# Kernel tuning notes

Hardware: AMD Instinct MI355X
Metric: run time of the kernel (lower is better)

## Reference

```python
import jax, jax.numpy as jnp
import numpy as np

SIZE = 4096
DOWN = SIZE // 16  # reduction_factor = 16 -> 256
N_TASKS = 16
BATCH = 2048
INIT_STD = 0.01


def setup_inputs() -> dict:
    key = jax.random.key(0)
    k_x, k_t, k_wd, k_wu = jax.random.split(key, 4)
    x = jax.random.normal(k_x, (BATCH, SIZE), dtype=jnp.float32)
    task_id = jax.random.randint(k_t, (BATCH,), 0, N_TASKS)
    # Stacked per-task adapter params (init: normal(std=0.01) weights, zero bias)
    Wd = jax.random.normal(k_wd, (N_TASKS, SIZE, DOWN), dtype=jnp.float32) * INIT_STD
    bd = jnp.zeros((N_TASKS, DOWN), dtype=jnp.float32)
    Wu = jax.random.normal(k_wu, (N_TASKS, DOWN, SIZE), dtype=jnp.float32) * INIT_STD
    bu = jnp.zeros((N_TASKS, SIZE), dtype=jnp.float32)
    return {"x": x, "task_id": task_id, "Wd": Wd, "bd": bd, "Wu": Wu, "bu": bu}


def reference(x, task_id, Wd, bd, Wu, bu):
    # Down-projection for all tasks, then select each sample's routed task.
    # [B, T, DOWN] is small (B*T*256), cheaper than gathering [B, SIZE, DOWN] weights.
    down_all = jnp.einsum('bd,tdh->bth', x, Wd) + bd[None]
    down = jnp.take_along_axis(down_all, task_id[:, None, None], axis=1)[:, 0]  # [B, DOWN]
    act = jax.nn.silu(down)
    # Up-projection for all tasks, select routed task. [B, T, SIZE]
    up_all = jnp.einsum('bh,thd->btd', act, Wu) + bu[None]
    up = jnp.take_along_axis(up_all, task_id[:, None, None], axis=1)[:, 0]  # [B, SIZE]
    return x + up  # residual=True (default)
```

## Files before the change

### kernel.cpp

```cpp
#include <hip/hip_runtime.h>

#define BATCH 2048
#define SIZE 4096
#define DOWN 256
#define NTASK 16
#define KC 16
#define KCHUNK (SIZE / KC)

typedef _Float16 half8 __attribute__((ext_vector_type(8)));
typedef float floatx4 __attribute__((ext_vector_type(4)));

__device__ __forceinline__ int imin(int a, int b) { return a < b ? a : b; }
__device__ __forceinline__ int uswz(int n) { return n ^ ((n >> 3) & 7); }

__global__ __launch_bounds__(256) void sort_kernel(const int* __restrict__ task_id,
                                                   int* __restrict__ taskOff,
                                                   int* __restrict__ sortedIdx,
                                                   int* __restrict__ taskOfPos) {
    __shared__ int cnt[NTASK];
    __shared__ int base[NTASK + 1];
    __shared__ int cur[NTASK];
    int tid = threadIdx.x;
    if (tid < NTASK) cnt[tid] = 0;
    __syncthreads();
    for (int i = tid; i < BATCH; i += 256) atomicAdd(&cnt[task_id[i]], 1);
    __syncthreads();
    if (tid == 0) {
        int s = 0;
        for (int t = 0; t < NTASK; t++) { base[t] = s; s += cnt[t]; }
        base[NTASK] = s;
    }
    __syncthreads();
    if (tid < NTASK) { cur[tid] = base[tid]; taskOff[tid] = base[tid]; }
    if (tid == 0) taskOff[NTASK] = BATCH;
    __syncthreads();
    for (int i = tid; i < BATCH; i += 256) {
        int t = task_id[i];
        int p = atomicAdd(&cur[t], 1);
        sortedIdx[p] = i;
        taskOfPos[p] = t;
    }
}

__global__ __launch_bounds__(256, 2) void gemm1_kernel(const float* __restrict__ x,
                                                       const float* __restrict__ Wd,
                                                       const int* __restrict__ taskOff,
                                                       const int* __restrict__ sortedIdx,
                                                       _Float16* __restrict__ partial) {
    int task = blockIdx.x >> 1, z = blockIdx.x & 1, kc = blockIdx.y;
    int rowStart = taskOff[task];
    int nrows = taskOff[task + 1] - rowStart;
    if (nrows <= 0) return;

    __shared__ half8 A_lds[8][65];
    __shared__ half8 B_lds[8][256];

    int tid = threadIdx.x;
    int wave = tid >> 6, lane = tid & 63, quad = lane >> 4, l15 = lane & 15;
    int kbase0 = kc * KCHUNK;
    const float* Wdt = Wd + (size_t)task * SIZE * DOWN;

    int bswz[4];
#pragma unroll
    for (int i = 0; i < 4; i++) bswz[i] = uswz(wave * 64 + i * 16 + l15);

    for (int r0 = z * 64; r0 < nrows; r0 += 128) {
        floatx4 acc[4][4];
#pragma unroll
        for (int mi = 0; mi < 4; mi++)
#pragma unroll
            for (int ni = 0; ni < 4; ni++) acc[mi][ni] = (floatx4){0.f, 0.f, 0.f, 0.f};

        int arow = tid >> 2;
        int asrc = sortedIdx[rowStart + imin(r0 + arow, nrows - 1)];
        const float* xrow = x + (size_t)asrc * SIZE;

        for (int kb = 0; kb < KCHUNK; kb += 64) {
            int kglob = kbase0 + kb;
            floatx4 fa[2][2];
#pragma unroll
            for (int j = 0; j < 2; j++) {
                int kg = ((tid & 3) << 1) | j;
                const float* src = xrow + kglob + kg * 8;
                fa[j][0] = *(const floatx4*)(src);
                fa[j][1] = *(const floatx4*)(src + 4);
            }
            floatx4 fb[2][8];
#pragma unroll
            for (int s = 0; s < 2; s++) {
                int kg = s * 4 + wave;
                const float* src = Wdt + (size_t)(kglob + kg * 8) * DOWN + lane * 4;
#pragma unroll
                for (int j = 0; j < 8; j++) fb[s][j] = *(const floatx4*)(src + (size_t)j * DOWN);
            }
            __syncthreads();
#pragma unroll
            for (int j = 0; j < 2; j++) {
                int kg = ((tid & 3) << 1) | j;
                half8 h;
                h[0] = (_Float16)fa[j][0][0]; h[1] = (_Float16)fa[j][0][1];
                h[2] = (_Float16)fa[j][0][2]; h[3] = (_Float16)fa[j][0][3];
                h[4] = (_Float16)fa[j][1][0]; h[5] = (_Float16)fa[j][1][1];
                h[6] = (_Float16)fa[j][1][2]; h[7] = (_Float16)fa[j][1][3];
                A_lds[kg][arow] = h;
            }
#pragma unroll
            for (int s = 0; s < 2; s++) {
                int kg = s * 4 + wave;
#pragma unroll
                for (int i = 0; i < 4; i++) {
                    half8 h;
#pragma unroll
                    for (int j = 0; j < 8; j++) h[j] = (_Float16)fb[s][j][i];
                    B_lds[kg][uswz(lane * 4 + i)] = h;
                }
            }
            __syncthreads();
#pragma unroll
            for (int ks = 0; ks < 2; ks++) {
                int kg = ks * 4 + quad;
                half8 a[4], b[4];
#pragma unroll
                for (int i = 0; i < 4; i++) a[i] = A_lds[kg][i * 16 + l15];
#pragma unroll
                for (int i = 0; i < 4; i++) b[i] = B_lds[kg][bswz[i]];
#pragma unroll
                for (int mi = 0; mi < 4; mi++)
#pragma unroll
                    for (int ni = 0; ni < 4; ni++)
                        acc[mi][ni] = __builtin_amdgcn_mfma_f32_16x16x32_f16(
                            a[mi], b[ni], acc[mi][ni], 0, 0, 0);
            }
        }
#pragma unroll
        for (int mi = 0; mi < 4; mi++) {
#pragma unroll
            for (int reg = 0; reg < 4; reg++) {
                int r = r0 + mi * 16 + quad * 4 + reg;
                if (r < nrows) {
                    size_t rowoff = ((size_t)kc * BATCH + (rowStart + r)) * DOWN;
#pragma unroll
                    for (int ni = 0; ni < 4; ni++) {
                        int h = wave * 64 + ni * 16 + l15;
                        partial[rowoff + h] = (_Float16)acc[mi][ni][reg];
                    }
                }
            }
        }
    }
}

__global__ __launch_bounds__(256) void silu_kernel(const _Float16* __restrict__ partial,
                                                   const float* __restrict__ bd,
                                                   const int* __restrict__ taskOfPos,
                                                   _Float16* __restrict__ act) {
    int idx = blockIdx.x * 256 + threadIdx.x;
    int s = idx >> 5;
    int h = (idx & 31) * 8;
    int t = taskOfPos[s];
    floatx4 b0 = *(const floatx4*)(bd + t * DOWN + h);
    floatx4 b1 = *(const floatx4*)(bd + t * DOWN + h + 4);
    float v[8];
    v[0] = b0[0]; v[1] = b0[1]; v[2] = b0[2]; v[3] = b0[3];
    v[4] = b1[0]; v[5] = b1[1]; v[6] = b1[2]; v[7] = b1[3];
#pragma unroll
    for (int kc = 0; kc < KC; kc++) {
        half8 p = *(const half8*)(partial + ((size_t)kc * BATCH + s) * DOWN + h);
#pragma unroll
        for (int j = 0; j < 8; j++) v[j] += (float)p[j];
    }
    half8 o;
#pragma unroll
    for (int j = 0; j < 8; j++) {
        float sv = v[j] / (1.0f + __expf(-v[j]));
        o[j] = (_Float16)sv;
    }
    *(half8*)(act + (size_t)s * DOWN + h) = o;
}

__global__ __launch_bounds__(256, 2) void gemm2_kernel(const _Float16* __restrict__ act,
                                                       const float* __restrict__ Wu,
                                                       const float* __restrict__ bu,
                                                       const float* __restrict__ x,
                                                       const int* __restrict__ taskOff,
                                                       const int* __restrict__ sortedIdx,
                                                       float* __restrict__ out) {
    int nt = blockIdx.x, task = blockIdx.y;
    int rowStart = taskOff[task];
    int nrows = taskOff[task + 1] - rowStart;
    if (nrows <= 0) return;

    __shared__ half8 A_lds[8][129];
    __shared__ half8 B_lds[8][128];

    int tid = threadIdx.x;
    int wave = tid >> 6, lane = tid & 63, quad = lane >> 4, l15 = lane & 15;
    int wm = wave >> 1, wn = wave & 1;
    int ncol0 = nt * 128;
    const float* Wut = Wu + (size_t)task * DOWN * SIZE;

    int bswz[4];
#pragma unroll
    for (int i = 0; i < 4; i++) bswz[i] = uswz(wn * 64 + i * 16 + l15);
    int kgB = tid >> 5, nfB = tid & 31;

    for (int r0 = 0; r0 < nrows; r0 += 128) {
        floatx4 acc[4][4];
#pragma unroll
        for (int mi = 0; mi < 4; mi++)
#pragma unroll
            for (int ni = 0; ni < 4; ni++) acc[mi][ni] = (floatx4){0.f, 0.f, 0.f, 0.f};

        int arow = tid >> 1;
        int s_a = rowStart + imin(r0 + arow, nrows - 1);
        const _Float16* actrow = act + (size_t)s_a * DOWN;

        for (int kb = 0; kb < DOWN; kb += 64) {
            half8 ha[4];
#pragma unroll
            for (int j = 0; j < 4; j++) {
                int kg = ((tid & 1) << 2) | j;
                ha[j] = *(const half8*)(actrow + kb + kg * 8);
            }
            floatx4 fb[8];
            const float* src = Wut + (size_t)(kb + kgB * 8) * SIZE + ncol0 + nfB * 4;
#pragma unroll
            for (int j = 0; j < 8; j++) fb[j] = *(const floatx4*)(src + (size_t)j * SIZE);
            __syncthreads();
#pragma unroll
            for (int j = 0; j < 4; j++) {
                int kg = ((tid & 1) << 2) | j;
                A_lds[kg][arow] = ha[j];
            }
#pragma unroll
            for (int i = 0; i < 4; i++) {
                half8 h;
#pragma unroll
                for (int j = 0; j < 8; j++) h[j] = (_Float16)fb[j][i];
                B_lds[kgB][uswz(nfB * 4 + i)] = h;
            }
            __syncthreads();
#pragma unroll
            for (int ks = 0; ks < 2; ks++) {
                int kg = ks * 4 + quad;
                half8 a[4], b[4];
#pragma unroll
                for (int i = 0; i < 4; i++) a[i] = A_lds[kg][wm * 64 + i * 16 + l15];
#pragma unroll
                for (int i = 0; i < 4; i++) b[i] = B_lds[kg][bswz[i]];
#pragma unroll
                for (int mi = 0; mi < 4; mi++)
#pragma unroll
                    for (int ni = 0; ni < 4; ni++)
                        acc[mi][ni] = __builtin_amdgcn_mfma_f32_16x16x32_f16(
                            a[mi], b[ni], acc[mi][ni], 0, 0, 0);
            }
        }
#pragma unroll
        for (int mi = 0; mi < 4; mi++) {
#pragma unroll
            for (int reg = 0; reg < 4; reg++) {
                int r = r0 + wm * 64 + mi * 16 + quad * 4 + reg;
                if (r < nrows) {
                    int b = sortedIdx[rowStart + r];
                    const float* xr = x + (size_t)b * SIZE;
                    float* outr = out + (size_t)b * SIZE;
#pragma unroll
                    for (int ni = 0; ni < 4; ni++) {
                        int n = ncol0 + wn * 64 + ni * 16 + l15;
                        outr[n] = acc[mi][ni][reg] + bu[task * SIZE + n] + xr[n];
                    }
                }
            }
        }
    }
}

extern "C" void kernel_launch(void* const* d_in, const int* in_sizes, int n_in,
                              void* d_out, int out_size, void* d_ws, size_t ws_size,
                              hipStream_t stream) {
    const float* x       = (const float*)d_in[0];
    const int*   task_id = (const int*)d_in[1];
    const float* Wd      = (const float*)d_in[2];
    const float* bd      = (const float*)d_in[3];
    const float* Wu      = (const float*)d_in[4];
    const float* bu      = (const float*)d_in[5];
    float* out = (float*)d_out;

    _Float16* partial = (_Float16*)d_out;
    _Float16* act     = (_Float16*)d_ws;
    int* taskOff   = (int*)(act + (size_t)BATCH * DOWN);
    int* sortedIdx = taskOff + 32;
    int* taskOfPos = sortedIdx + BATCH;

    sort_kernel<<<1, 256, 0, stream>>>(task_id, taskOff, sortedIdx, taskOfPos);
    gemm1_kernel<<<dim3(NTASK * 2, KC), 256, 0, stream>>>(x, Wd, taskOff, sortedIdx, partial);
    silu_kernel<<<(BATCH * DOWN / 8) / 256, 256, 0, stream>>>(partial, bd, taskOfPos, act);
    gemm2_kernel<<<dim3(SIZE / 128, NTASK), 256, 0, stream>>>(act, Wu, bu, x, taskOff,
                                                              sortedIdx, out);
}
```

Before: 236.1 us.

## Stage full A tile in LDS once and give each wave private B tiles without barriers

Both GEMMs now load the whole row tile of activations (the x chunk or act rows) into LDS once per row block, instead of reloading it every k step. Each wave converts and stores its own slice of B into a private LDS region, so the two __syncthreads per k step are removed. gemm2 switches to 64-row by 256-column tiles with a row split across two blocks, matching gemm1. The cost is more registers per thread (16 float4 loads per k step) and the loss of the old XOR swizzle on B, which may bring back LDS bank conflicts.

```diff
diff --git a/kernel.cpp b/kernel.cpp
--- a/kernel.cpp
+++ b/kernel.cpp
@@ -8,10 +8,10 @@
 #define KCHUNK (SIZE / KC)
 
 typedef _Float16 half8 __attribute__((ext_vector_type(8)));
+typedef _Float16 half4 __attribute__((ext_vector_type(4)));
 typedef float floatx4 __attribute__((ext_vector_type(4)));
 
 __device__ __forceinline__ int imin(int a, int b) { return a < b ? a : b; }
-__device__ __forceinline__ int uswz(int n) { return n ^ ((n >> 3) & 7); }
 
 __global__ __launch_bounds__(256) void sort_kernel(const int* __restrict__ task_id,
                                                    int* __restrict__ taskOff,
@@ -52,78 +52,64 @@
     int nrows = taskOff[task + 1] - rowStart;
     if (nrows <= 0) return;
 
-    __shared__ half8 A_lds[8][65];
-    __shared__ half8 B_lds[8][256];
+    __shared__ half8 A_lds[32][64];
+    __shared__ half8 B_lds[4][64][8];
 
     int tid = threadIdx.x;
     int wave = tid >> 6, lane = tid & 63, quad = lane >> 4, l15 = lane & 15;
-    int kbase0 = kc * KCHUNK;
+    int kbase = kc * KCHUNK;
     const float* Wdt = Wd + (size_t)task * SIZE * DOWN;
-
-    int bswz[4];
-#pragma unroll
-    for (int i = 0; i < 4; i++) bswz[i] = uswz(wave * 64 + i * 16 + l15);
+    int arow = tid >> 2, ac = tid & 3;
 
     for (int r0 = z * 64; r0 < nrows; r0 += 128) {
+        __syncthreads();
+        {
+            int asrc = sortedIdx[rowStart + imin(r0 + arow, nrows - 1)];
+            const float* xr = x + (size_t)asrc * SIZE + kbase;
+            floatx4 f[16];
+#pragma unroll
+            for (int i = 0; i < 16; i++)
+                f[i] = *(const floatx4*)(xr + i * 16 + ac * 4);
+#pragma unroll
+            for (int i = 0; i < 16; i++) {
+                half4 h;
+                h[0] = (_Float16)f[i][0]; h[1] = (_Float16)f[i][1];
+                h[2] = (_Float16)f[i][2]; h[3] = (_Float16)f[i][3];
+                int kg = i * 2 + (ac >> 1);
+                *((half4*)(&A_lds[kg][arow]) + (ac & 1)) = h;
+            }
+        }
+        __syncthreads();
+
         floatx4 acc[4][4];
 #pragma unroll
         for (int mi = 0; mi < 4; mi++)
 #pragma unroll
             for (int ni = 0; ni < 4; ni++) acc[mi][ni] = (floatx4){0.f, 0.f, 0.f, 0.f};
 
-        int arow = tid >> 2;
-        int asrc = sortedIdx[rowStart + imin(r0 + arow, nrows - 1)];
-        const float* xrow = x + (size_t)asrc * SIZE;
-
         for (int kb = 0; kb < KCHUNK; kb += 64) {
-            int kglob = kbase0 + kb;
-            floatx4 fa[2][2];
-#pragma unroll
-            for (int j = 0; j < 2; j++) {
-                int kg = ((tid & 3) << 1) | j;
-                const float* src = xrow + kglob + kg * 8;
-                fa[j][0] = *(const floatx4*)(src);
-                fa[j][1] = *(const floatx4*)(src + 4);
-            }
-            floatx4 fb[2][8];
-#pragma unroll
-            for (int s = 0; s < 2; s++) {
-                int kg = s * 4 + wave;
-                const float* src = Wdt + (size_t)(kglob + kg * 8) * DOWN + lane * 4;
-#pragma unroll
-                for (int j = 0; j < 8; j++) fb[s][j] = *(const floatx4*)(src + (size_t)j * DOWN);
-            }
-            __syncthreads();
-#pragma unroll
-            for (int j = 0; j < 2; j++) {
-                int kg = ((tid & 3) << 1) | j;
-                half8 h;
-                h[0] = (_Float16)fa[j][0][0]; h[1] = (_Float16)fa[j][0][1];
-                h[2] = (_Float16)fa[j][0][2]; h[3] = (_Float16)fa[j][0][3];
-                h[4] = (_Float16)fa[j][1][0]; h[5] = (_Float16)fa[j][1][1];
-                h[6] = (_Float16)fa[j][1][2]; h[7] = (_Float16)fa[j][1][3];
-                A_lds[kg][arow] = h;
-            }
-#pragma unroll
-            for (int s = 0; s < 2; s++) {
-                int kg = s * 4 + wave;
-#pragma unroll
-                for (int i = 0; i < 4; i++) {
+            floatx4 fb[16];
+            const float* bs =
+                Wdt + (size_t)(kbase + kb + quad * 16) * DOWN + wave * 64 + l15 * 4;
+#pragma unroll
+            for (int j = 0; j < 16; j++) fb[j] = *(const floatx4*)(bs + (size_t)j * DOWN);
+#pragma unroll
+            for (int g = 0; g < 2; g++)
+#pragma unroll
+                for (int n2 = 0; n2 < 4; n2++) {
                     half8 h;
 #pragma unroll
-                    for (int j = 0; j < 8; j++) h[j] = (_Float16)fb[s][j][i];
-                    B_lds[kg][uswz(lane * 4 + i)] = h;
-                }
-            }
-            __syncthreads();
+                    for (int e = 0; e < 8; e++) h[e] = (_Float16)fb[g * 8 + e][n2];
+                    B_lds[wave][l15 * 4 + n2][quad * 2 + g] = h;
+                }
 #pragma unroll
             for (int ks = 0; ks < 2; ks++) {
-                int kg = ks * 4 + quad;
+                int kg = (kb >> 3) + ks * 4 + quad;
                 half8 a[4], b[4];
 #pragma unroll
                 for (int i = 0; i < 4; i++) a[i] = A_lds[kg][i * 16 + l15];
 #pragma unroll
-                for (int i = 0; i < 4; i++) b[i] = B_lds[kg][bswz[i]];
+                for (int i = 0; i < 4; i++) b[i] = B_lds[wave][i * 16 + l15][ks * 4 + quad];
 #pragma unroll
                 for (int mi = 0; mi < 4; mi++)
 #pragma unroll
@@ -185,69 +171,62 @@
                                                        const int* __restrict__ taskOff,
                                                        const int* __restrict__ sortedIdx,
                                                        float* __restrict__ out) {
-    int nt = blockIdx.x, task = blockIdx.y;
+    int nt = blockIdx.x >> 1, z = blockIdx.x & 1, task = blockIdx.y;
     int rowStart = taskOff[task];
     int nrows = taskOff[task + 1] - rowStart;
     if (nrows <= 0) return;
 
-    __shared__ half8 A_lds[8][129];
-    __shared__ half8 B_lds[8][128];
+    __shared__ half8 A_lds[32][64];
+    __shared__ half8 B_lds[4][64][8];
 
     int tid = threadIdx.x;
     int wave = tid >> 6, lane = tid & 63, quad = lane >> 4, l15 = lane & 15;
-    int wm = wave >> 1, wn = wave & 1;
-    int ncol0 = nt * 128;
+    int ncol0 = nt * 256;
     const float* Wut = Wu + (size_t)task * DOWN * SIZE;
-
-    int bswz[4];
-#pragma unroll
-    for (int i = 0; i < 4; i++) bswz[i] = uswz(wn * 64 + i * 16 + l15);
-    int kgB = tid >> 5, nfB = tid & 31;
-
-    for (int r0 = 0; r0 < nrows; r0 += 128) {
+    int arow = tid >> 2, ac = tid & 3;
+
+    for (int r0 = z * 64; r0 < nrows; r0 += 128) {
+        __syncthreads();
+        {
+            int s_a = rowStart + imin(r0 + arow, nrows - 1);
+            const _Float16* ar = act + (size_t)s_a * DOWN;
+#pragma unroll
+            for (int j = 0; j < 8; j++) {
+                int kg = j * 4 + ac;
+                A_lds[kg][arow] = *(const half8*)(ar + kg * 8);
+            }
+        }
+        __syncthreads();
+
         floatx4 acc[4][4];
 #pragma unroll
         for (int mi = 0; mi < 4; mi++)
 #pragma unroll
             for (int ni = 0; ni < 4; ni++) acc[mi][ni] = (floatx4){0.f, 0.f, 0.f, 0.f};
 
-        int arow = tid >> 1;
-        int s_a = rowStart + imin(r0 + arow, nrows - 1);
-        const _Float16* actrow = act + (size_t)s_a * DOWN;
-
         for (int kb = 0; kb < DOWN; kb += 64) {
-            half8 ha[4];
-#pragma unroll
-            for (int j = 0; j < 4; j++) {
-                int kg = ((tid & 1) << 2) | j;
-                ha[j] = *(const half8*)(actrow + kb + kg * 8);
-            }
-            floatx4 fb[8];
-            const float* src = Wut + (size_t)(kb + kgB * 8) * SIZE + ncol0 + nfB * 4;
-#pragma unroll
-            for (int j = 0; j < 8; j++) fb[j] = *(const floatx4*)(src + (size_t)j * SIZE);
-            __syncthreads();
-#pragma unroll
-            for (int j = 0; j < 4; j++) {
-                int kg = ((tid & 1) << 2) | j;
-                A_lds[kg][arow] = ha[j];
-            }
-#pragma unroll
-            for (int i = 0; i < 4; i++) {
-                half8 h;
-#pragma unroll
-                for (int j = 0; j < 8; j++) h[j] = (_Float16)fb[j][i];
-                B_lds[kgB][uswz(nfB * 4 + i)] = h;
-            }
-            __syncthreads();
+            floatx4 fb[16];
+            const float* bs =
+                Wut + (size_t)(kb + quad * 16) * SIZE + ncol0 + wave * 64 + l15 * 4;
+#pragma unroll
+            for (int j = 0; j < 16; j++) fb[j] = *(const floatx4*)(bs + (size_t)j * SIZE);
+#pragma unroll
+            for (int g = 0; g < 2; g++)
+#pragma unroll
+                for (int n2 = 0; n2 < 4; n2++) {
+                    half8 h;
+#pragma unroll
+                    for (int e = 0; e < 8; e++) h[e] = (_Float16)fb[g * 8 + e][n2];
+                    B_lds[wave][l15 * 4 + n2][quad * 2 + g] = h;
+                }
 #pragma unroll
             for (int ks = 0; ks < 2; ks++) {
-                int kg = ks * 4 + quad;
+                int kg = (kb >> 3) + ks * 4 + quad;
                 half8 a[4], b[4];
 #pragma unroll
-                for (int i = 0; i < 4; i++) a[i] = A_lds[kg][wm * 64 + i * 16 + l15];
-#pragma unroll
-                for (int i = 0; i < 4; i++) b[i] = B_lds[kg][bswz[i]];
+                for (int i = 0; i < 4; i++) a[i] = A_lds[kg][i * 16 + l15];
+#pragma unroll
+                for (int i = 0; i < 4; i++) b[i] = B_lds[wave][i * 16 + l15][ks * 4 + quad];
 #pragma unroll
                 for (int mi = 0; mi < 4; mi++)
 #pragma unroll
@@ -260,14 +239,14 @@
         for (int mi = 0; mi < 4; mi++) {
 #pragma unroll
             for (int reg = 0; reg < 4; reg++) {
-                int r = r0 + wm * 64 + mi * 16 + quad * 4 + reg;
+                int r = r0 + mi * 16 + quad * 4 + reg;
                 if (r < nrows) {
                     int b = sortedIdx[rowStart + r];
                     const float* xr = x + (size_t)b * SIZE;
                     float* outr = out + (size_t)b * SIZE;
 #pragma unroll
                     for (int ni = 0; ni < 4; ni++) {
-                        int n = ncol0 + wn * 64 + ni * 16 + l15;
+                        int n = ncol0 + wave * 64 + ni * 16 + l15;
                         outr[n] = acc[mi][ni][reg] + bu[task * SIZE + n] + xr[n];
                     }
                 }
@@ -296,6 +275,6 @@
     sort_kernel<<<1, 256, 0, stream>>>(task_id, taskOff, sortedIdx, taskOfPos);
     gemm1_kernel<<<dim3(NTASK * 2, KC), 256, 0, stream>>>(x, Wd, taskOff, sortedIdx, partial);
     silu_kernel<<<(BATCH * DOWN / 8) / 256, 256, 0, stream>>>(partial, bd, taskOfPos, act);
-    gemm2_kernel<<<dim3(SIZE / 128, NTASK), 256, 0, stream>>>(act, Wu, bu, x, taskOff,
-                                                              sortedIdx, out);
-}
+    gemm2_kernel<<<dim3(32, NTASK), 256, 0, stream>>>(act, Wu, bu, x, taskOff,
+                                                      sortedIdx, out);
+}
```

New measurement: 254.5 us. 1.08x slower.

## Pre-convert weights to packed fp16 tiles and double-buffer GEMMs with async LDS loads

Applied to the files above, without the earlier changes.

Adds a prep kernel that folds the sort into block 0 and converts Wd and Wu from fp32 into fp16 tiles laid out to match the MFMA operand order. The weights go into the workspace and the output buffer. Both GEMMs then stream these tiles straight into double-buffered LDS with global_load_lds, overlapping the next tile's load with the current MFMAs, and occupancy is raised to 3. This removes per-block re-conversion of the weights and halves their read bytes in the GEMMs. The cost is an extra full pass over the weights each call, plus a larger workspace requirement with an fp32 fallback path when the workspace is too small.

```diff
diff --git a/kernel.cpp b/kernel.cpp
--- a/kernel.cpp
+++ b/kernel.cpp
@@ -11,12 +11,17 @@
 typedef float floatx4 __attribute__((ext_vector_type(4)));
 
 __device__ __forceinline__ int imin(int a, int b) { return a < b ? a : b; }
-__device__ __forceinline__ int uswz(int n) { return n ^ ((n >> 3) & 7); }
-
-__global__ __launch_bounds__(256) void sort_kernel(const int* __restrict__ task_id,
-                                                   int* __restrict__ taskOff,
-                                                   int* __restrict__ sortedIdx,
-                                                   int* __restrict__ taskOfPos) {
+
+__device__ __forceinline__ void async16(void* lds, const void* g) {
+    __builtin_amdgcn_global_load_lds((const __attribute__((address_space(1))) unsigned int*)g,
+                                     (__attribute__((address_space(3))) unsigned int*)lds,
+                                     16, 0, 0);
+}
+
+__device__ __forceinline__ void sort_body(const int* __restrict__ task_id,
+                                          int* __restrict__ taskOff,
+                                          int* __restrict__ sortedIdx,
+                                          int* __restrict__ taskOfPos) {
     __shared__ int cnt[NTASK];
     __shared__ int base[NTASK + 1];
     __shared__ int cur[NTASK];
@@ -42,8 +47,62 @@
     }
 }
 
-__global__ __launch_bounds__(256, 2) void gemm1_kernel(const float* __restrict__ x,
-                                                       const float* __restrict__ Wd,
+__global__ __launch_bounds__(256) void sort_kernel(const int* __restrict__ task_id,
+                                                   int* __restrict__ taskOff,
+                                                   int* __restrict__ sortedIdx,
+                                                   int* __restrict__ taskOfPos) {
+    sort_body(task_id, taskOff, sortedIdx, taskOfPos);
+}
+
+__global__ __launch_bounds__(256) void prep_kernel(const int* __restrict__ task_id,
+                                                   int* __restrict__ taskOff,
+                                                   int* __restrict__ sortedIdx,
+                                                   int* __restrict__ taskOfPos,
+                                                   const float* __restrict__ Wd,
+                                                   const float* __restrict__ Wu,
+                                                   _Float16* __restrict__ Wd16,
+                                                   _Float16* __restrict__ Wu16) {
+    int b = blockIdx.x;
+    if (b == 0) {
+        sort_body(task_id, taskOff, sortedIdx, taskOfPos);
+        return;
+    }
+    int tid = threadIdx.x, w = tid >> 6, lane = tid & 63;
+    const float* src;
+    _Float16* dst;
+    size_t rstride;
+    if (b <= 1024) {
+        int i = b - 1, t = i >> 6, ks = i & 63;
+        src = Wd + ((size_t)t * SIZE + ks * 64) * DOWN;
+        dst = Wd16 + (size_t)(t * 64 + ks) * 16384;
+        rstride = DOWN;
+    } else {
+        int i = b - 1025, t = i >> 6, nt = (i >> 2) & 15, ks = i & 3;
+        src = Wu + ((size_t)t * DOWN + ks * 64) * SIZE + nt * 256;
+        dst = Wu16 + (size_t)((t * 16 + nt) * 4 + ks) * 16384;
+        rstride = SIZE;
+    }
+#pragma unroll
+    for (int kk = 0; kk < 2; kk++) {
+        int kg = w * 2 + kk;
+        float f[8][4];
+#pragma unroll
+        for (int e = 0; e < 8; e++)
+#pragma unroll
+            for (int j = 0; j < 4; j++)
+                f[e][j] = src[(size_t)(kg * 8 + e) * rstride + j * 64 + lane];
+#pragma unroll
+        for (int j = 0; j < 4; j++) {
+            half8 h;
+#pragma unroll
+            for (int e = 0; e < 8; e++) h[e] = (_Float16)f[e][j];
+            *(half8*)(dst + (size_t)(kg * 256 + j * 64 + lane) * 8) = h;
+        }
+    }
+}
+
+__global__ __launch_bounds__(256, 3) void gemm1_kernel(const float* __restrict__ x,
+                                                       const _Float16* __restrict__ Wd16,
                                                        const int* __restrict__ taskOff,
                                                        const int* __restrict__ sortedIdx,
                                                        _Float16* __restrict__ partial) {
@@ -52,85 +111,81 @@
     int nrows = taskOff[task + 1] - rowStart;
     if (nrows <= 0) return;
 
-    __shared__ half8 A_lds[8][65];
-    __shared__ half8 B_lds[8][256];
+    __shared__ floatx4 Af[2][64][8];
+    __shared__ half8 Bp[2][4][256];
 
     int tid = threadIdx.x;
     int wave = tid >> 6, lane = tid & 63, quad = lane >> 4, l15 = lane & 15;
-    int kbase0 = kc * KCHUNK;
-    const float* Wdt = Wd + (size_t)task * SIZE * DOWN;
-
-    int bswz[4];
-#pragma unroll
-    for (int i = 0; i < 4; i++) bswz[i] = uswz(wave * 64 + i * 16 + l15);
+    int arow = tid >> 2, c4 = tid & 3;
+    int kcbase = kc * KCHUNK;
 
     for (int r0 = z * 64; r0 < nrows; r0 += 128) {
+        int asrc = sortedIdx[rowStart + imin(r0 + arow, nrows - 1)];
+        const float* xrow = x + (size_t)asrc * SIZE + kcbase;
+
+        {
+            const char* tb = (const char*)Wd16 +
+                             (((size_t)task * 64 + kc * 4) << 15);
+#pragma unroll
+            for (int i = 0; i < 4; i++)
+                async16((char*)(&Bp[0][0][0]) + (wave * 4 + i) * 1024,
+                        tb + (wave * 4 + i) * 1024 + lane * 16);
+            floatx4 f0 = *(const floatx4*)(xrow + c4 * 8);
+            floatx4 f1 = *(const floatx4*)(xrow + c4 * 8 + 4);
+            Af[0][arow][(c4 * 2) ^ (arow & 7)] = f0;
+            Af[0][arow][(c4 * 2 + 1) ^ (arow & 7)] = f1;
+        }
+        __syncthreads();
+
         floatx4 acc[4][4];
 #pragma unroll
         for (int mi = 0; mi < 4; mi++)
 #pragma unroll
             for (int ni = 0; ni < 4; ni++) acc[mi][ni] = (floatx4){0.f, 0.f, 0.f, 0.f};
 
-        int arow = tid >> 2;
-        int asrc = sortedIdx[rowStart + imin(r0 + arow, nrows - 1)];
-        const float* xrow = x + (size_t)asrc * SIZE;
-
-        for (int kb = 0; kb < KCHUNK; kb += 64) {
-            int kglob = kbase0 + kb;
-            floatx4 fa[2][2];
-#pragma unroll
-            for (int j = 0; j < 2; j++) {
-                int kg = ((tid & 3) << 1) | j;
-                const float* src = xrow + kglob + kg * 8;
-                fa[j][0] = *(const floatx4*)(src);
-                fa[j][1] = *(const floatx4*)(src + 4);
-            }
-            floatx4 fb[2][8];
-#pragma unroll
-            for (int s = 0; s < 2; s++) {
-                int kg = s * 4 + wave;
-                const float* src = Wdt + (size_t)(kglob + kg * 8) * DOWN + lane * 4;
-#pragma unroll
-                for (int j = 0; j < 8; j++) fb[s][j] = *(const floatx4*)(src + (size_t)j * DOWN);
+        int buf = 0;
+        for (int ts = 0; ts < 8; ts++) {
+            floatx4 f0, f1;
+            if (ts < 7) {
+                int tn = ts + 1;
+                const char* tb = (const char*)Wd16 +
+                                 (((size_t)task * 64 + kc * 4 + (tn >> 1)) << 15) +
+                                 ((size_t)(tn & 1) << 14);
+#pragma unroll
+                for (int i = 0; i < 4; i++)
+                    async16((char*)(&Bp[buf ^ 1][0][0]) + (wave * 4 + i) * 1024,
+                            tb + (wave * 4 + i) * 1024 + lane * 16);
+                f0 = *(const floatx4*)(xrow + tn * 32 + c4 * 8);
+                f1 = *(const floatx4*)(xrow + tn * 32 + c4 * 8 + 4);
+            }
+            half8 a[4], bfr[4];
+#pragma unroll
+            for (int mi = 0; mi < 4; mi++) {
+                int row = mi * 16 + l15, s7 = row & 7;
+                floatx4 u0 = Af[buf][row][(quad * 2) ^ s7];
+                floatx4 u1 = Af[buf][row][(quad * 2 + 1) ^ s7];
+                half8 h;
+                h[0] = (_Float16)u0[0]; h[1] = (_Float16)u0[1];
+                h[2] = (_Float16)u0[2]; h[3] = (_Float16)u0[3];
+                h[4] = (_Float16)u1[0]; h[5] = (_Float16)u1[1];
+                h[6] = (_Float16)u1[2]; h[7] = (_Float16)u1[3];
+                a[mi] = h;
+            }
+#pragma unroll
+            for (int ni = 0; ni < 4; ni++)
+                bfr[ni] = Bp[buf][quad][wave * 64 + ni * 16 + l15];
+#pragma unroll
+            for (int mi = 0; mi < 4; mi++)
+#pragma unroll
+                for (int ni = 0; ni < 4; ni++)
+                    acc[mi][ni] = __builtin_amdgcn_mfma_f32_16x16x32_f16(
+                        a[mi], bfr[ni], acc[mi][ni], 0, 0, 0);
+            if (ts < 7) {
+                Af[buf ^ 1][arow][(c4 * 2) ^ (arow & 7)] = f0;
+                Af[buf ^ 1][arow][(c4 * 2 + 1) ^ (arow & 7)] = f1;
             }
             __syncthreads();
-#pragma unroll
-            for (int j = 0; j < 2; j++) {
-                int kg = ((tid & 3) << 1) | j;
-                half8 h;
-                h[0] = (_Float16)fa[j][0][0]; h[1] = (_Float16)fa[j][0][1];
-                h[2] = (_Float16)fa[j][0][2]; h[3] = (_Float16)fa[j][0][3];
-                h[4] = (_Float16)fa[j][1][0]; h[5] = (_Float16)fa[j][1][1];
-                h[6] = (_Float16)fa[j][1][2]; h[7] = (_Float16)fa[j][1][3];
-                A_lds[kg][arow] = h;
-            }
-#pragma unroll
-            for (int s = 0; s < 2; s++) {
-                int kg = s * 4 + wave;
-#pragma unroll
-                for (int i = 0; i < 4; i++) {
-                    half8 h;
-#pragma unroll
-                    for (int j = 0; j < 8; j++) h[j] = (_Float16)fb[s][j][i];
-                    B_lds[kg][uswz(lane * 4 + i)] = h;
-                }
-            }
-            __syncthreads();
-#pragma unroll
-            for (int ks = 0; ks < 2; ks++) {
-                int kg = ks * 4 + quad;
-                half8 a[4], b[4];
-#pragma unroll
-                for (int i = 0; i < 4; i++) a[i] = A_lds[kg][i * 16 + l15];
-#pragma unroll
-                for (int i = 0; i < 4; i++) b[i] = B_lds[kg][bswz[i]];
-#pragma unroll
-                for (int mi = 0; mi < 4; mi++)
-#pragma unroll
-                    for (int ni = 0; ni < 4; ni++)
-                        acc[mi][ni] = __builtin_amdgcn_mfma_f32_16x16x32_f16(
-                            a[mi], b[ni], acc[mi][ni], 0, 0, 0);
-            }
+            buf ^= 1;
         }
 #pragma unroll
         for (int mi = 0; mi < 4; mi++) {
@@ -178,96 +233,283 @@
     *(half8*)(act + (size_t)s * DOWN + h) = o;
 }
 
-__global__ __launch_bounds__(256, 2) void gemm2_kernel(const _Float16* __restrict__ act,
-                                                       const float* __restrict__ Wu,
+__global__ __launch_bounds__(256, 3) void gemm2_kernel(const _Float16* __restrict__ act,
+                                                       const _Float16* __restrict__ Wu16,
                                                        const float* __restrict__ bu,
                                                        const float* __restrict__ x,
                                                        const int* __restrict__ taskOff,
                                                        const int* __restrict__ sortedIdx,
                                                        float* __restrict__ out) {
-    int nt = blockIdx.x, task = blockIdx.y;
+    int nt = blockIdx.x >> 1, z = blockIdx.x & 1, task = blockIdx.y;
     int rowStart = taskOff[task];
     int nrows = taskOff[task + 1] - rowStart;
     if (nrows <= 0) return;
 
-    __shared__ half8 A_lds[8][129];
-    __shared__ half8 B_lds[8][128];
+    __shared__ half8 Ah[2][64][4];
+    __shared__ half8 Bp[2][4][256];
 
     int tid = threadIdx.x;
     int wave = tid >> 6, lane = tid & 63, quad = lane >> 4, l15 = lane & 15;
-    int wm = wave >> 1, wn = wave & 1;
-    int ncol0 = nt * 128;
-    const float* Wut = Wu + (size_t)task * DOWN * SIZE;
-
-    int bswz[4];
-#pragma unroll
-    for (int i = 0; i < 4; i++) bswz[i] = uswz(wn * 64 + i * 16 + l15);
-    int kgB = tid >> 5, nfB = tid & 31;
-
-    for (int r0 = 0; r0 < nrows; r0 += 128) {
+    int ncol0 = nt * 256;
+
+    for (int r0 = z * 64; r0 < nrows; r0 += 128) {
+        int ar = wave * 16 + (lane >> 2);
+        const _Float16* asrc_row =
+            act + (size_t)(rowStart + imin(r0 + ar, nrows - 1)) * DOWN +
+            ((lane & 3) ^ (ar & 3)) * 8;
+
+        {
+            const char* tb = (const char*)Wu16 +
+                             (((size_t)(task * 16 + nt) * 4) << 15);
+#pragma unroll
+            for (int i = 0; i < 4; i++)
+                async16((char*)(&Bp[0][0][0]) + (wave * 4 + i) * 1024,
+                        tb + (wave * 4 + i) * 1024 + lane * 16);
+            async16((char*)(&Ah[0][0][0]) + wave * 1024, asrc_row);
+        }
+        __syncthreads();
+
         floatx4 acc[4][4];
 #pragma unroll
         for (int mi = 0; mi < 4; mi++)
 #pragma unroll
             for (int ni = 0; ni < 4; ni++) acc[mi][ni] = (floatx4){0.f, 0.f, 0.f, 0.f};
 
-        int arow = tid >> 1;
-        int s_a = rowStart + imin(r0 + arow, nrows - 1);
-        const _Float16* actrow = act + (size_t)s_a * DOWN;
-
-        for (int kb = 0; kb < DOWN; kb += 64) {
-            half8 ha[4];
-#pragma unroll
-            for (int j = 0; j < 4; j++) {
-                int kg = ((tid & 1) << 2) | j;
-                ha[j] = *(const half8*)(actrow + kb + kg * 8);
-            }
-            floatx4 fb[8];
-            const float* src = Wut + (size_t)(kb + kgB * 8) * SIZE + ncol0 + nfB * 4;
-#pragma unroll
-            for (int j = 0; j < 8; j++) fb[j] = *(const floatx4*)(src + (size_t)j * SIZE);
+        int buf = 0;
+        for (int ts = 0; ts < 8; ts++) {
+            if (ts < 7) {
+                int tn = ts + 1;
+                const char* tb = (const char*)Wu16 +
+                                 (((size_t)(task * 16 + nt) * 4 + (tn >> 1)) << 15) +
+                                 ((size_t)(tn & 1) << 14);
+#pragma unroll
+                for (int i = 0; i < 4; i++)
+                    async16((char*)(&Bp[buf ^ 1][0][0]) + (wave * 4 + i) * 1024,
+                            tb + (wave * 4 + i) * 1024 + lane * 16);
+                async16((char*)(&Ah[buf ^ 1][0][0]) + wave * 1024, asrc_row + tn * 32);
+            }
+            half8 a[4], bfr[4];
+#pragma unroll
+            for (int mi = 0; mi < 4; mi++) {
+                int row = mi * 16 + l15;
+                a[mi] = Ah[buf][row][quad ^ (row & 3)];
+            }
+#pragma unroll
+            for (int ni = 0; ni < 4; ni++)
+                bfr[ni] = Bp[buf][quad][wave * 64 + ni * 16 + l15];
+#pragma unroll
+            for (int mi = 0; mi < 4; mi++)
+#pragma unroll
+                for (int ni = 0; ni < 4; ni++)
+                    acc[mi][ni] = __builtin_amdgcn_mfma_f32_16x16x32_f16(
+                        a[mi], bfr[ni], acc[mi][ni], 0, 0, 0);
             __syncthreads();
-#pragma unroll
-            for (int j = 0; j < 4; j++) {
-                int kg = ((tid & 1) << 2) | j;
-                A_lds[kg][arow] = ha[j];
-            }
-#pragma unroll
-            for (int i = 0; i < 4; i++) {
-                half8 h;
-#pragma unroll
-                for (int j = 0; j < 8; j++) h[j] = (_Float16)fb[j][i];
-                B_lds[kgB][uswz(nfB * 4 + i)] = h;
-            }
-            __syncthreads();
-#pragma unroll
-            for (int ks = 0; ks < 2; ks++) {
-                int kg = ks * 4 + quad;
-                half8 a[4], b[4];
-#pragma unroll
-                for (int i = 0; i < 4; i++) a[i] = A_lds[kg][wm * 64 + i * 16 + l15];
-#pragma unroll
-                for (int i = 0; i < 4; i++) b[i] = B_lds[kg][bswz[i]];
-#pragma unroll
-                for (int mi = 0; mi < 4; mi++)
-#pragma unroll
-                    for (int ni = 0; ni < 4; ni++)
-                        acc[mi][ni] = __builtin_amdgcn_mfma_f32_16x16x32_f16(
-                            a[mi], b[ni], acc[mi][ni], 0, 0, 0);
-            }
+            buf ^= 1;
         }
 #pragma unroll
         for (int mi = 0; mi < 4; mi++) {
 #pragma unroll
             for (int reg = 0; reg < 4; reg++) {
-                int r = r0 + wm * 64 + mi * 16 + quad * 4 + reg;
+                int r = r0 + mi * 16 + quad * 4 + reg;
                 if (r < nrows) {
                     int b = sortedIdx[rowStart + r];
                     const float* xr = x + (size_t)b * SIZE;
                     float* outr = out + (size_t)b * SIZE;
 #pragma unroll
                     for (int ni = 0; ni < 4; ni++) {
-                        int n = ncol0 + wn * 64 + ni * 16 + l15;
+                        int n = ncol0 + wave * 64 + ni * 16 + l15;
+                        outr[n] = acc[mi][ni][reg] + bu[task * SIZE + n] + xr[n];
+                    }
+                }
+            }
+        }
+    }
+}
+
+__global__ __launch_bounds__(256, 2) void gemm1_fb(const float* __restrict__ x,
+                                                   const float* __restrict__ Wd,
+                                                   const int* __restrict__ taskOff,
+                                                   const int* __restrict__ sortedIdx,
+                                                   _Float16* __restrict__ partial) {
+    int task = blockIdx.x >> 1, z = blockIdx.x & 1, kc = blockIdx.y;
+    int rowStart = taskOff[task];
+    int nrows = taskOff[task + 1] - rowStart;
+    if (nrows <= 0) return;
+    __shared__ half8 A_lds[8][65];
+    __shared__ half8 B_lds[8][256];
+    int tid = threadIdx.x;
+    int wave = tid >> 6, lane = tid & 63, quad = lane >> 4, l15 = lane & 15;
+    int kbase0 = kc * KCHUNK;
+    const float* Wdt = Wd + (size_t)task * SIZE * DOWN;
+    int uswz[4];
+#pragma unroll
+    for (int i = 0; i < 4; i++) {
+        int n = wave * 64 + i * 16 + l15;
+        uswz[i] = n ^ ((n >> 3) & 7);
+    }
+    for (int r0 = z * 64; r0 < nrows; r0 += 128) {
+        floatx4 acc[4][4];
+#pragma unroll
+        for (int mi = 0; mi < 4; mi++)
+#pragma unroll
+            for (int ni = 0; ni < 4; ni++) acc[mi][ni] = (floatx4){0.f, 0.f, 0.f, 0.f};
+        int arow = tid >> 2;
+        int asrc = sortedIdx[rowStart + imin(r0 + arow, nrows - 1)];
+        const float* xrow = x + (size_t)asrc * SIZE;
+        for (int kb = 0; kb < KCHUNK; kb += 64) {
+            int kglob = kbase0 + kb;
+            floatx4 fa[2][2];
+#pragma unroll
+            for (int j = 0; j < 2; j++) {
+                int kg = ((tid & 3) << 1) | j;
+                const float* src = xrow + kglob + kg * 8;
+                fa[j][0] = *(const floatx4*)(src);
+                fa[j][1] = *(const floatx4*)(src + 4);
+            }
+            floatx4 fb[2][8];
+#pragma unroll
+            for (int s = 0; s < 2; s++) {
+                int kg = s * 4 + wave;
+                const float* src = Wdt + (size_t)(kglob + kg * 8) * DOWN + lane * 4;
+#pragma unroll
+                for (int j = 0; j < 8; j++) fb[s][j] = *(const floatx4*)(src + (size_t)j * DOWN);
+            }
+            __syncthreads();
+#pragma unroll
+            for (int j = 0; j < 2; j++) {
+                int kg = ((tid & 3) << 1) | j;
+                half8 h;
+                h[0] = (_Float16)fa[j][0][0]; h[1] = (_Float16)fa[j][0][1];
+                h[2] = (_Float16)fa[j][0][2]; h[3] = (_Float16)fa[j][0][3];
+                h[4] = (_Float16)fa[j][1][0]; h[5] = (_Float16)fa[j][1][1];
+                h[6] = (_Float16)fa[j][1][2]; h[7] = (_Float16)fa[j][1][3];
+                A_lds[kg][arow] = h;
+            }
+#pragma unroll
+            for (int s = 0; s < 2; s++) {
+                int kg = s * 4 + wave;
+#pragma unroll
+                for (int i = 0; i < 4; i++) {
+                    half8 h;
+#pragma unroll
+                    for (int j = 0; j < 8; j++) h[j] = (_Float16)fb[s][j][i];
+                    int n = lane * 4 + i;
+                    B_lds[kg][n ^ ((n >> 3) & 7)] = h;
+                }
+            }
+            __syncthreads();
+#pragma unroll
+            for (int ks = 0; ks < 2; ks++) {
+                int kg = ks * 4 + quad;
+                half8 a[4], b[4];
+#pragma unroll
+                for (int i = 0; i < 4; i++) a[i] = A_lds[kg][i * 16 + l15];
+#pragma unroll
+                for (int i = 0; i < 4; i++) b[i] = B_lds[kg][uswz[i]];
+#pragma unroll
+                for (int mi = 0; mi < 4; mi++)
+#pragma unroll
+                    for (int ni = 0; ni < 4; ni++)
+                        acc[mi][ni] = __builtin_amdgcn_mfma_f32_16x16x32_f16(
+                            a[mi], b[ni], acc[mi][ni], 0, 0, 0);
+            }
+        }
+#pragma unroll
+        for (int mi = 0; mi < 4; mi++) {
+#pragma unroll
+            for (int reg = 0; reg < 4; reg++) {
+                int r = r0 + mi * 16 + quad * 4 + reg;
+                if (r < nrows) {
+                    size_t rowoff = ((size_t)kc * BATCH + (rowStart + r)) * DOWN;
+#pragma unroll
+                    for (int ni = 0; ni < 4; ni++) {
+                        int h = wave * 64 + ni * 16 + l15;
+                        partial[rowoff + h] = (_Float16)acc[mi][ni][reg];
+                    }
+                }
+            }
+        }
+    }
+}
+
+__global__ __launch_bounds__(256, 2) void gemm2_fb(const _Float16* __restrict__ act,
+                                                   const float* __restrict__ Wu,
+                                                   const float* __restrict__ bu,
+                                                   const float* __restrict__ x,
+                                                   const int* __restrict__ taskOff,
+                                                   const int* __restrict__ sortedIdx,
+                                                   float* __restrict__ out) {
+    int nt = blockIdx.x >> 1, z = blockIdx.x & 1, task = blockIdx.y;
+    int rowStart = taskOff[task];
+    int nrows = taskOff[task + 1] - rowStart;
+    if (nrows <= 0) return;
+    __shared__ half8 A_lds[32][64];
+    __shared__ half8 B_lds[4][64][8];
+    int tid = threadIdx.x;
+    int wave = tid >> 6, lane = tid & 63, quad = lane >> 4, l15 = lane & 15;
+    int ncol0 = nt * 256;
+    const float* Wut = Wu + (size_t)task * DOWN * SIZE;
+    int arow = tid >> 2, ac = tid & 3;
+    for (int r0 = z * 64; r0 < nrows; r0 += 128) {
+        __syncthreads();
+        {
+            int s_a = rowStart + imin(r0 + arow, nrows - 1);
+            const _Float16* ar = act + (size_t)s_a * DOWN;
+#pragma unroll
+            for (int j = 0; j < 8; j++) {
+                int kg = j * 4 + ac;
+                A_lds[kg][arow] = *(const half8*)(ar + kg * 8);
+            }
+        }
+        __syncthreads();
+        floatx4 acc[4][4];
+#pragma unroll
+        for (int mi = 0; mi < 4; mi++)
+#pragma unroll
+            for (int ni = 0; ni < 4; ni++) acc[mi][ni] = (floatx4){0.f, 0.f, 0.f, 0.f};
+        for (int kb = 0; kb < DOWN; kb += 64) {
+            floatx4 fb[16];
+            const float* bs =
+                Wut + (size_t)(kb + quad * 16) * SIZE + ncol0 + wave * 64 + l15 * 4;
+#pragma unroll
+            for (int j = 0; j < 16; j++) fb[j] = *(const floatx4*)(bs + (size_t)j * SIZE);
+#pragma unroll
+            for (int g = 0; g < 2; g++)
+#pragma unroll
+                for (int n2 = 0; n2 < 4; n2++) {
+                    half8 h;
+#pragma unroll
+                    for (int e = 0; e < 8; e++) h[e] = (_Float16)fb[g * 8 + e][n2];
+                    B_lds[wave][l15 * 4 + n2][quad * 2 + g] = h;
+                }
+#pragma unroll
+            for (int ks = 0; ks < 2; ks++) {
+                int kg = (kb >> 3) + ks * 4 + quad;
+                half8 a[4], b[4];
+#pragma unroll
+                for (int i = 0; i < 4; i++) a[i] = A_lds[kg][i * 16 + l15];
+#pragma unroll
+                for (int i = 0; i < 4; i++) b[i] = B_lds[wave][i * 16 + l15][ks * 4 + quad];
+#pragma unroll
+                for (int mi = 0; mi < 4; mi++)
+#pragma unroll
+                    for (int ni = 0; ni < 4; ni++)
+                        acc[mi][ni] = __builtin_amdgcn_mfma_f32_16x16x32_f16(
+                            a[mi], b[ni], acc[mi][ni], 0, 0, 0);
+            }
+        }
+#pragma unroll
+        for (int mi = 0; mi < 4; mi++) {
+#pragma unroll
+            for (int reg = 0; reg < 4; reg++) {
+                int r = r0 + mi * 16 + quad * 4 + reg;
+                if (r < nrows) {
+                    int b = sortedIdx[rowStart + r];
+                    const float* xr = x + (size_t)b * SIZE;
+                    float* outr = out + (size_t)b * SIZE;
+#pragma unroll
+                    for (int ni = 0; ni < 4; ni++) {
+                        int n = ncol0 + wave * 64 + ni * 16 + l15;
                         outr[n] = acc[mi][ni][reg] + bu[task * SIZE + n] + xr[n];
                     }
                 }
@@ -287,15 +529,37 @@
     const float* bu      = (const float*)d_in[5];
     float* out = (float*)d_out;
 
-    _Float16* partial = (_Float16*)d_out;
-    _Float16* act     = (_Float16*)d_ws;
-    int* taskOff   = (int*)(act + (size_t)BATCH * DOWN);
-    int* sortedIdx = taskOff + 32;
-    int* taskOfPos = sortedIdx + BATCH;
-
-    sort_kernel<<<1, 256, 0, stream>>>(task_id, taskOff, sortedIdx, taskOfPos);
-    gemm1_kernel<<<dim3(NTASK * 2, KC), 256, 0, stream>>>(x, Wd, taskOff, sortedIdx, partial);
-    silu_kernel<<<(BATCH * DOWN / 8) / 256, 256, 0, stream>>>(partial, bd, taskOfPos, act);
-    gemm2_kernel<<<dim3(SIZE / 128, NTASK), 256, 0, stream>>>(act, Wu, bu, x, taskOff,
-                                                              sortedIdx, out);
-}
+    size_t need = ((size_t)49 << 20) + 16384;
+    if (ws_size >= need) {
+        char* wsb = (char*)d_ws;
+        _Float16* partial = (_Float16*)wsb;
+        _Float16* Wu16    = (_Float16*)(wsb + ((size_t)16 << 20));
+        _Float16* act     = (_Float16*)(wsb + ((size_t)48 << 20));
+        int* taskOff   = (int*)(wsb + ((size_t)49 << 20));
+        int* sortedIdx = taskOff + 32;
+        int* taskOfPos = sortedIdx + BATCH;
+        _Float16* Wd16 = (_Float16*)d_out;
+
+        prep_kernel<<<2049, 256, 0, stream>>>(task_id, taskOff, sortedIdx, taskOfPos,
+                                              Wd, Wu, Wd16, Wu16);
+        gemm1_kernel<<<dim3(NTASK * 2, KC), 256, 0, stream>>>(x, Wd16, taskOff,
+                                                              sortedIdx, partial);
+        silu_kernel<<<(BATCH * DOWN / 8) / 256, 256, 0, stream>>>(partial, bd,
+                                                                  taskOfPos, act);
+        gemm2_kernel<<<dim3(32, NTASK), 256, 0, stream>>>(act, Wu16, bu, x, taskOff,
+                                                          sortedIdx, out);
+    } else {
+        _Float16* partial = (_Float16*)d_out;
+        _Float16* act     = (_Float16*)d_ws;
+        int* taskOff   = (int*)(act + (size_t)BATCH * DOWN);
+        int* sortedIdx = taskOff + 32;
+        int* taskOfPos = sortedIdx + BATCH;
+        sort_kernel<<<1, 256, 0, stream>>>(task_id, taskOff, sortedIdx, taskOfPos);
+        gemm1_fb<<<dim3(NTASK * 2, KC), 256, 0, stream>>>(x, Wd, taskOff, sortedIdx,
+                                                          partial);
+        silu_kernel<<<(BATCH * DOWN / 8) / 256, 256, 0, stream>>>(partial, bd,
+                                                                  taskOfPos, act);
+        gemm2_fb<<<dim3(32, NTASK), 256, 0, stream>>>(act, Wu, bu, x, taskOff,
+                                                      sortedIdx, out);
+    }
+}
```

Result: slower. 278.1 us (+17.8%).
